# Kernel optimization log

Hardware: AMD Instinct MI355X
Metric: run time of the kernel (lower is better)

The kernel has to match this reference:

```python
import jax, jax.numpy as jnp
import numpy as np

EMB_DIM, D_H, BSZ, SEQ = 2048, 128, 4, 4096
HALF = D_H // 2


def apply_rope(x, sin, cos):
    # x: [b, s, d]; sin/cos: [s, d//2]; interleaved-pair rotation
    b, s, d = x.shape
    xr = x.reshape(b, s, d // 2, 2)
    x0, x1 = xr[..., 0], xr[..., 1]
    r0 = x0 * cos - x1 * sin
    r1 = x1 * cos + x0 * sin
    return jnp.stack([r0, r1], axis=-1).reshape(b, s, d)


def setup_inputs() -> dict:
    key = jax.random.key(0)
    kx, kq, kk, kv = jax.random.split(key, 4)
    x = jax.random.normal(kx, (BSZ, SEQ, EMB_DIM), dtype=jnp.float32)
    # causal mask (1 = attend, 0 = masked), matching mask[q,:] slicing in source
    mask = jnp.tril(jnp.ones((SEQ, SEQ), dtype=jnp.int32))
    # standard RoPE angle tables: [seq, d_h//2]
    inv_freq = 1.0 / (10000.0 ** (jnp.arange(HALF, dtype=jnp.float32) / HALF))
    angles = jnp.arange(SEQ, dtype=jnp.float32)[:, None] * inv_freq[None, :]
    sin, cos = jnp.sin(angles), jnp.cos(angles)
    scale = 1.0 / np.sqrt(EMB_DIM)
    W_Q = jax.random.normal(kq, (EMB_DIM, D_H), dtype=jnp.float32) * scale
    W_K = jax.random.normal(kk, (EMB_DIM, D_H), dtype=jnp.float32) * scale
    W_V = jax.random.normal(kv, (EMB_DIM, D_H), dtype=jnp.float32) * scale
    return {"x": x, "mask": mask, "sin": sin, "cos": cos,
            "W_Q": W_Q, "W_K": W_K, "W_V": W_V}


def reference(x, mask, sin, cos, W_Q, W_V, W_K):
    # QKV projections
    Q = apply_rope(x @ W_Q, sin, cos)  # [b, s, d_h]
    K = apply_rope(x @ W_K, sin, cos)  # [b, s, d_h]
    V = x @ W_V                        # [b, s, d_h]
    # The source's chunked loop is exactly full masked attention over all K/V.
    scores = jnp.einsum('bqd,bkd->bqk', Q, K) / jnp.sqrt(jnp.float32(D_H))
    scores = jnp.where(mask[None, :, :] == 0, -jnp.inf, scores)
    attn = jax.nn.softmax(scores, axis=-1)
    return jnp.einsum('bqk,bkd->bqd', attn, V)
```

## Files before the change

kernel.cpp:

```cpp
#include <hip/hip_runtime.h>
#include <stdint.h>
#include <stddef.h>

typedef __bf16 bf16;
typedef __bf16 bf16x8 __attribute__((ext_vector_type(8)));
typedef float f32x4 __attribute__((ext_vector_type(4)));
typedef unsigned int uint32x2 __attribute__((ext_vector_type(2)));
typedef unsigned int uint32x4 __attribute__((ext_vector_type(4)));

typedef const __attribute__((address_space(1))) uint32_t GU32;
typedef __attribute__((address_space(3))) uint32_t LU32;

__device__ __forceinline__ f32x4 mfma16(bf16x8 a, bf16x8 b, f32x4 c) {
  return __builtin_amdgcn_mfma_f32_16x16x32_bf16(a, b, c, 0, 0, 0);
}
__device__ __forceinline__ void gload16(const void* g, void* l) {
  __builtin_amdgcn_global_load_lds((GU32*)g, (LU32*)l, 16, 0, 0);
}

__global__ void k_prep(const float* __restrict__ Wq, const float* __restrict__ Wk,
                       const float* __restrict__ Wv, bf16* __restrict__ Wct) {
  int t = blockIdx.x * 256 + threadIdx.x;
  int n = t >> 11, k = t & 2047;
  const float* s = (n < 128) ? Wq : (n < 256) ? Wk : Wv;
  Wct[t] = (bf16)s[k * 128 + (n & 127)];
}

__global__ __launch_bounds__(256, 3) void k_proj(
    const float* __restrict__ x, const float* __restrict__ sint, const float* __restrict__ cost,
    const bf16* __restrict__ Wct, bf16* __restrict__ Qg, bf16* __restrict__ Kg,
    bf16* __restrict__ Vtg) {
  __shared__ __align__(16) uint8_t smem[49152];
  const int tid = threadIdx.x;
  const int lane = tid & 63, w = tid >> 6;
  const int l15 = lane & 15, l16 = lane >> 4;
  const int nb = blockIdx.x % 3, mb = blockIdx.x / 3;
  const int wm = w >> 1, wn = w & 1;
  const int arow = tid >> 2, aj = tid & 3;

  f32x4 acc[2][4] = {};
  f32x4 areg[4];

  const float* abase = x + (size_t)(mb * 64 + arow) * 2048 + aj * 16;

  auto stageB = [&](int buf, int ks) {
    uint8_t* bbm = smem + buf * 24576 + 8192;
    int k0 = ks * 64;
#pragma unroll
    for (int i = 0; i < 4; ++i) {
      int L = i * 4096 + tid * 16;
      int n = L >> 7, cp = (L >> 4) & 7;
      int cc = cp ^ (n & 7);
      const uint8_t* src = (const uint8_t*)Wct + (((nb * 128 + n) * 2048 + k0 + cc * 8) << 1);
      gload16(src, bbm + i * 4096 + w * 1024);
    }
  };
  auto loadA = [&](int ks) {
    const f32x4* p = (const f32x4*)(abase + ks * 64);
#pragma unroll
    for (int i = 0; i < 4; ++i) areg[i] = p[i];
  };
  auto writeA = [&](int buf) {
    uint8_t* ab = smem + buf * 24576;
#pragma unroll
    for (int h = 0; h < 2; ++h) {
      union { bf16 v[8]; uint32x4 u; } pk;
#pragma unroll
      for (int e = 0; e < 8; ++e) pk.v[e] = (bf16)areg[h * 2 + (e >> 2)][e & 3];
      int c = aj * 2 + h;
      *(uint32x4*)(ab + arow * 128 + (((c ^ (arow & 7)) & 7) << 4)) = pk.u;
    }
  };
  auto compute = [&](int buf) {
    uint8_t* ab = smem + buf * 24576;
    uint8_t* bbm = ab + 8192;
#pragma unroll
    for (int kk = 0; kk < 2; ++kk) {
      bf16x8 af[2], bv[4];
#pragma unroll
      for (int mt = 0; mt < 2; ++mt) {
        int ml = wm * 32 + mt * 16 + l15;
        af[mt] = *(const bf16x8*)(ab + ml * 128 + (((kk * 4 + l16) ^ (ml & 7)) << 4));
      }
#pragma unroll
      for (int nt = 0; nt < 4; ++nt) {
        int nl = wn * 64 + nt * 16 + l15;
        bv[nt] = *(const bf16x8*)(bbm + nl * 128 + (((kk * 4 + l16) ^ (nl & 7)) << 4));
      }
#pragma unroll
      for (int mt = 0; mt < 2; ++mt)
#pragma unroll
        for (int nt = 0; nt < 4; ++nt)
          acc[mt][nt] = mfma16(af[mt], bv[nt], acc[mt][nt]);
    }
  };

  stageB(0, 0);
  loadA(0);
  writeA(0);
  __syncthreads();
  for (int ks = 0; ks < 32; ++ks) {
    int cur = ks & 1;
    if (ks + 1 < 32) { stageB(cur ^ 1, ks + 1); loadA(ks + 1); }
    compute(cur);
    if (ks + 1 < 32) writeA(cur ^ 1);
    __syncthreads();
  }

  const int bb = mb >> 6;
#pragma unroll
  for (int mt = 0; mt < 2; ++mt) {
    int gm = mb * 64 + wm * 32 + mt * 16 + l16 * 4;
    int s0 = gm & 4095;
#pragma unroll
    for (int nt = 0; nt < 4; ++nt) {
      int jcol = nb * 128 + wn * 64 + nt * 16 + l15;
      f32x4 v = acc[mt][nt];
      if (jcol < 256) {
        int p = (jcol & 127) >> 1;
        bool even = ((jcol & 1) == 0);
#pragma unroll
        for (int r = 0; r < 4; ++r) {
          float pv = __shfl_xor(v[r], 1);
          int s = s0 + r;
          float cs = cost[s * 64 + p], sn = sint[s * 64 + p];
          float nv = even ? (v[r] * cs - pv * sn) : (v[r] * cs + pv * sn);
          bf16 hb = (bf16)nv;
          if (jcol < 128) Qg[((size_t)(bb << 12) + s) * 128 + jcol] = hb;
          else            Kg[((size_t)(bb << 12) + s) * 128 + jcol - 128] = hb;
        }
      } else {
        int d = jcol - 256;
        union { bf16 h[4]; uint32x2 u; } pk;
#pragma unroll
        for (int r = 0; r < 4; ++r) pk.h[r] = (bf16)v[r];
        *(uint32x2*)((uint8_t*)Vtg + (((size_t)(bb << 7) + d) * 4096 + s0) * 2) = pk.u;
      }
    }
  }
}

__global__ __launch_bounds__(256, 2) void k_attn(
    const bf16* __restrict__ Qg, const bf16* __restrict__ Kg, const bf16* __restrict__ Vtg,
    float* __restrict__ PO, float* __restrict__ ML) {
  __shared__ __align__(16) uint8_t smem[81920];
  const int tid = threadIdx.x;
  const int lane = tid & 63, w = tid >> 6;
  const int l15 = lane & 15, l16 = lane >> 4;

  int gid = blockIdx.x;
  int b = gid / 80, rr = gid % 80;
  int j, c;
  if (rr < 8)       { j = rr;                 c = 0; }
  else if (rr < 24) { j = 8 + ((rr - 8) >> 1);  c = (rr - 8) & 1; }
  else if (rr < 48) { j = 16 + (rr - 24) / 3;   c = (rr - 24) % 3; }
  else              { j = 24 + ((rr - 48) >> 2); c = (rr - 48) & 3; }

  const int q0w = j * 128 + w * 32;
  const int kv_lo = c * 1024;
  const int kv_hi = min((c + 1) * 1024, (j + 1) * 128);
  const int T = (kv_hi - kv_lo) >> 6;

  bf16x8 qf[2][4];
#pragma unroll
  for (int qt = 0; qt < 2; ++qt)
#pragma unroll
    for (int kk = 0; kk < 4; ++kk)
      qf[qt][kk] = *(const bf16x8*)(Qg + ((size_t)(b << 12) + q0w + qt * 16 + l15) * 128 + kk * 32 + l16 * 8);

  f32x4 o[2][8] = {};
  float m_r[2] = {-1e30f, -1e30f};
  float l_r[2] = {0.f, 0.f};
  uint8_t* pb = smem + 65536 + w * 4096;

  auto stage = [&](int t) {
    uint8_t* kb = smem + (t & 1) * 32768;
    uint8_t* vb = kb + 16384;
    int kv0 = kv_lo + t * 64;
#pragma unroll
    for (int i = 0; i < 4; ++i) {
      int L = i * 4096 + tid * 16;
      {
        int kv = L >> 8, cp = (L >> 4) & 15, cc = cp ^ (kv & 7);
        const uint8_t* src = (const uint8_t*)Kg + ((size_t)((b << 12) + kv0 + kv) << 8) + (cc << 4);
        gload16(src, kb + i * 4096 + w * 1024);
      }
      {
        int d = L >> 7, cp = (L >> 4) & 7, cc = cp ^ (d & 7);
        const uint8_t* src = (const uint8_t*)Vtg + ((size_t)(((b << 7) + d) << 12) + kv0 + (cc << 3)) * 2;
        gload16(src, vb + i * 4096 + w * 1024);
      }
    }
  };

  stage(0);
  __syncthreads();

  for (int t = 0; t < T; ++t) {
    if (t + 1 < T) stage(t + 1);
    const int kv0 = kv_lo + t * 64;
    if (kv0 <= q0w + 31) {
      uint8_t* kb = smem + (t & 1) * 32768;
      uint8_t* vb = kb + 16384;
      f32x4 sfr[4][2] = {};
#pragma unroll
      for (int kk = 0; kk < 4; ++kk) {
#pragma unroll
        for (int kvt = 0; kvt < 4; ++kvt) {
          int kvl = kvt * 16 + l15;
          bf16x8 kf = *(const bf16x8*)(kb + (kvl << 8) + (((kk * 4 + l16) ^ (kvl & 7)) << 4));
#pragma unroll
          for (int qt = 0; qt < 2; ++qt)
            sfr[kvt][qt] = mfma16(kf, qf[qt][kk], sfr[kvt][qt]);
        }
      }
      const bool need_mask = (kv0 + 63 > q0w);
      const float scale = 0.08838834764831845f;
#pragma unroll
      for (int qt = 0; qt < 2; ++qt) {
        const int q = q0w + qt * 16 + l15;
        float pvv[4][4];
        float tmax = -1e30f;
#pragma unroll
        for (int kvt = 0; kvt < 4; ++kvt)
#pragma unroll
          for (int r = 0; r < 4; ++r) {
            float sv = sfr[kvt][qt][r] * scale;
            if (need_mask) {
              int kv = kv0 + kvt * 16 + l16 * 4 + r;
              if (kv > q) sv = -1e30f;
            }
            pvv[kvt][r] = sv;
            tmax = fmaxf(tmax, sv);
          }
        tmax = fmaxf(tmax, __shfl_xor(tmax, 16));
        tmax = fmaxf(tmax, __shfl_xor(tmax, 32));
        float mnew = fmaxf(m_r[qt], tmax);
        float corr = __expf(m_r[qt] - mnew);
        m_r[qt] = mnew;
        float rs = 0.f;
#pragma unroll
        for (int kvt = 0; kvt < 4; ++kvt)
#pragma unroll
          for (int r = 0; r < 4; ++r) {
            float p = __expf(pvv[kvt][r] - mnew);
            pvv[kvt][r] = p;
            rs += p;
          }
        rs += __shfl_xor(rs, 16);
        rs += __shfl_xor(rs, 32);
        l_r[qt] = l_r[qt] * corr + rs;
        const int qrow = qt * 16 + l15;
#pragma unroll
        for (int kvt = 0; kvt < 4; ++kvt) {
          union { bf16 h[4]; uint32x2 u; } pk;
#pragma unroll
          for (int r = 0; r < 4; ++r) pk.h[r] = (bf16)pvv[kvt][r];
          int kv2 = kvt * 32 + l16 * 8;
          *(uint32x2*)(pb + qrow * 128 + ((((kv2 >> 4) ^ (qrow & 7)) << 4) | (kv2 & 15))) = pk.u;
        }
#pragma unroll
        for (int r = 0; r < 4; ++r) {
          float cr = __shfl(corr, l16 * 4 + r);
#pragma unroll
          for (int dt = 0; dt < 8; ++dt) o[qt][dt][r] *= cr;
        }
      }
#pragma unroll
      for (int kvb = 0; kvb < 2; ++kvb) {
        bf16x8 pa[2];
#pragma unroll
        for (int qt = 0; qt < 2; ++qt) {
          int qrow = qt * 16 + l15;
          int kv2 = kvb * 64 + l16 * 16;
          pa[qt] = *(const bf16x8*)(pb + qrow * 128 + (((kv2 >> 4) ^ (qrow & 7)) << 4));
        }
#pragma unroll
        for (int dt = 0; dt < 8; ++dt) {
          int d = dt * 16 + l15;
          bf16x8 vf = *(const bf16x8*)(vb + (d << 7) + (((kvb * 4 + l16) ^ (d & 7)) << 4));
#pragma unroll
          for (int qt = 0; qt < 2; ++qt)
            o[qt][dt] = mfma16(pa[qt], vf, o[qt][dt]);
        }
      }
    }
    __syncthreads();
  }

  float* POb = PO + (size_t)((b * 32 + j) * 4 + c) * 16384;
#pragma unroll
  for (int qt = 0; qt < 2; ++qt)
#pragma unroll
    for (int dt = 0; dt < 8; ++dt)
#pragma unroll
      for (int r = 0; r < 4; ++r)
        POb[(w * 32 + qt * 16 + l16 * 4 + r) * 128 + dt * 16 + l15] = o[qt][dt][r];
  float* MLb = ML + (size_t)((b * 32 + j) * 4 + c) * 256;
  if (l16 == 0) {
#pragma unroll
    for (int qt = 0; qt < 2; ++qt) {
      MLb[w * 32 + qt * 16 + l15] = m_r[qt];
      MLb[128 + w * 32 + qt * 16 + l15] = l_r[qt];
    }
  }
}

__global__ void k_combine(const float* __restrict__ PO, const float* __restrict__ ML,
                          float* __restrict__ out) {
  int blk = blockIdx.x;
  int b = blk >> 5, j = blk & 31;
  int nc = 1 + (j >> 3);
  int t = threadIdx.x;
  int q = t >> 1, half = t & 1;
  const float* MLb = ML + (size_t)(b * 32 + j) * 4 * 256;
  float mv[4], lv[4];
  float ms = -1e30f;
  for (int cc = 0; cc < nc; ++cc) {
    mv[cc] = MLb[cc * 256 + q];
    lv[cc] = MLb[cc * 256 + 128 + q];
    ms = fmaxf(ms, mv[cc]);
  }
  float wgt[4];
  float den = 0.f;
  for (int cc = 0; cc < nc; ++cc) { wgt[cc] = __expf(mv[cc] - ms); den += wgt[cc] * lv[cc]; }
  float inv = 1.f / den;
  const float* POb = PO + (size_t)(b * 32 + j) * 4 * 16384 + q * 128 + half * 64;
  float* ob = out + ((size_t)(b << 12) + j * 128 + q) * 128 + half * 64;
  for (int d = 0; d < 64; d += 4) {
    f32x4 a = {0.f, 0.f, 0.f, 0.f};
    for (int cc = 0; cc < nc; ++cc) {
      f32x4 v = *(const f32x4*)(POb + cc * 16384 + d);
      a += v * wgt[cc];
    }
    a *= inv;
    *(f32x4*)(ob + d) = a;
  }
}

extern "C" void kernel_launch(void* const* d_in, const int* in_sizes, int n_in,
                              void* d_out, int out_size, void* d_ws, size_t ws_size,
                              hipStream_t stream) {
  const float* x = (const float*)d_in[0];
  const float* sint = (const float*)d_in[2];
  const float* cost = (const float*)d_in[3];
  const float* Wq = (const float*)d_in[4];
  const float* Wk = (const float*)d_in[5];
  const float* Wv = (const float*)d_in[6];
  uint8_t* ws = (uint8_t*)d_ws;

  bf16* Wct = (bf16*)(ws + 0x0);
  bf16* Qg  = (bf16*)(ws + 0x180000);
  bf16* Kg  = (bf16*)(ws + 0x580000);
  bf16* Vtg = (bf16*)(ws + 0x980000);
  float* PO = (float*)(ws + 0xD80000);
  float* ML = (float*)(ws + 0x2D80000);
  float* out = (float*)d_out;

  hipLaunchKernelGGL(k_prep, dim3(3072), dim3(256), 0, stream, Wq, Wk, Wv, Wct);
  hipLaunchKernelGGL(k_proj, dim3(768), dim3(256), 0, stream, x, sint, cost, Wct, Qg, Kg, Vtg);
  hipLaunchKernelGGL(k_attn, dim3(320), dim3(256), 0, stream, Qg, Kg, Vtg, PO, ML);
  hipLaunchKernelGGL(k_combine, dim3(128), dim3(256), 0, stream, PO, ML, out);
}
```

Measured before the change: 152.9 us.

## Widen projection N-tile to 192 columns and transpose weights via LDS

```diff
diff --git a/kernel.cpp b/kernel.cpp
--- a/kernel.cpp
+++ b/kernel.cpp
@@ -18,40 +18,61 @@
   __builtin_amdgcn_global_load_lds((GU32*)g, (LU32*)l, 16, 0, 0);
 }
 
-__global__ void k_prep(const float* __restrict__ Wq, const float* __restrict__ Wk,
-                       const float* __restrict__ Wv, bf16* __restrict__ Wct) {
-  int t = blockIdx.x * 256 + threadIdx.x;
-  int n = t >> 11, k = t & 2047;
-  const float* s = (n < 128) ? Wq : (n < 256) ? Wk : Wv;
-  Wct[t] = (bf16)s[k * 128 + (n & 127)];
-}
-
-__global__ __launch_bounds__(256, 3) void k_proj(
+__global__ __launch_bounds__(256) void k_prep(const float* __restrict__ Wq,
+                                              const float* __restrict__ Wk,
+                                              const float* __restrict__ Wv,
+                                              bf16* __restrict__ Wct) {
+  __shared__ float tile[64][65];
+  const int tid = threadIdx.x;
+  const int widx = blockIdx.x >> 6, rem = blockIdx.x & 63;
+  const int k0 = (rem >> 1) * 64, n0 = (rem & 1) * 64;
+  const float* W = (widx == 0) ? Wq : (widx == 1) ? Wk : Wv;
+  const int rg = tid >> 4, cq = tid & 15;
+#pragma unroll
+  for (int i = 0; i < 4; ++i) {
+    int krow = i * 16 + rg;
+    f32x4 v = *(const f32x4*)(W + (size_t)(k0 + krow) * 128 + n0 + cq * 4);
+#pragma unroll
+    for (int j = 0; j < 4; ++j) tile[krow][cq * 4 + j] = v[j];
+  }
+  __syncthreads();
+#pragma unroll
+  for (int i = 0; i < 4; ++i) {
+    int nrow = i * 16 + rg;
+    union { bf16 h[4]; uint32x2 u; } pk;
+#pragma unroll
+    for (int j = 0; j < 4; ++j) pk.h[j] = (bf16)tile[cq * 4 + j][nrow];
+    *(uint32x2*)(Wct + (size_t)(widx * 128 + n0 + nrow) * 2048 + k0 + cq * 4) = pk.u;
+  }
+}
+
+__global__ __launch_bounds__(256, 2) void k_proj(
     const float* __restrict__ x, const float* __restrict__ sint, const float* __restrict__ cost,
     const bf16* __restrict__ Wct, bf16* __restrict__ Qg, bf16* __restrict__ Kg,
     bf16* __restrict__ Vtg) {
-  __shared__ __align__(16) uint8_t smem[49152];
+  __shared__ __align__(16) uint8_t smem[65536];
   const int tid = threadIdx.x;
   const int lane = tid & 63, w = tid >> 6;
   const int l15 = lane & 15, l16 = lane >> 4;
-  const int nb = blockIdx.x % 3, mb = blockIdx.x / 3;
+  const int logical = (blockIdx.x & 7) * 64 + (blockIdx.x >> 3);
+  const int nb = logical & 1, mb = logical >> 1;
   const int wm = w >> 1, wn = w & 1;
   const int arow = tid >> 2, aj = tid & 3;
 
-  f32x4 acc[2][4] = {};
+  f32x4 acc[2][6] = {};
   f32x4 areg[4];
 
   const float* abase = x + (size_t)(mb * 64 + arow) * 2048 + aj * 16;
 
   auto stageB = [&](int buf, int ks) {
-    uint8_t* bbm = smem + buf * 24576 + 8192;
+    uint8_t* bbm = smem + buf * 32768 + 8192;
     int k0 = ks * 64;
 #pragma unroll
-    for (int i = 0; i < 4; ++i) {
+    for (int i = 0; i < 6; ++i) {
       int L = i * 4096 + tid * 16;
       int n = L >> 7, cp = (L >> 4) & 7;
       int cc = cp ^ (n & 7);
-      const uint8_t* src = (const uint8_t*)Wct + (((nb * 128 + n) * 2048 + k0 + cc * 8) << 1);
+      const uint8_t* src = (const uint8_t*)Wct + (((size_t)(nb * 192 + n) * 2048 + k0 + cc * 8) << 1);
       gload16(src, bbm + i * 4096 + w * 1024);
     }
   };
@@ -61,7 +82,7 @@
     for (int i = 0; i < 4; ++i) areg[i] = p[i];
   };
   auto writeA = [&](int buf) {
-    uint8_t* ab = smem + buf * 24576;
+    uint8_t* ab = smem + buf * 32768;
 #pragma unroll
     for (int h = 0; h < 2; ++h) {
       union { bf16 v[8]; uint32x4 u; } pk;
@@ -72,25 +93,25 @@
     }
   };
   auto compute = [&](int buf) {
-    uint8_t* ab = smem + buf * 24576;
+    uint8_t* ab = smem + buf * 32768;
     uint8_t* bbm = ab + 8192;
 #pragma unroll
     for (int kk = 0; kk < 2; ++kk) {
-      bf16x8 af[2], bv[4];
+      bf16x8 af[2], bv[6];
 #pragma unroll
       for (int mt = 0; mt < 2; ++mt) {
         int ml = wm * 32 + mt * 16 + l15;
         af[mt] = *(const bf16x8*)(ab + ml * 128 + (((kk * 4 + l16) ^ (ml & 7)) << 4));
       }
 #pragma unroll
-      for (int nt = 0; nt < 4; ++nt) {
-        int nl = wn * 64 + nt * 16 + l15;
+      for (int nt = 0; nt < 6; ++nt) {
+        int nl = wn * 96 + nt * 16 + l15;
         bv[nt] = *(const bf16x8*)(bbm + nl * 128 + (((kk * 4 + l16) ^ (nl & 7)) << 4));
       }
 #pragma unroll
       for (int mt = 0; mt < 2; ++mt)
 #pragma unroll
-        for (int nt = 0; nt < 4; ++nt)
+        for (int nt = 0; nt < 6; ++nt)
           acc[mt][nt] = mfma16(af[mt], bv[nt], acc[mt][nt]);
     }
   };
@@ -107,14 +128,13 @@
     __syncthreads();
   }
 
-  const int bb = mb >> 6;
 #pragma unroll
   for (int mt = 0; mt < 2; ++mt) {
     int gm = mb * 64 + wm * 32 + mt * 16 + l16 * 4;
-    int s0 = gm & 4095;
-#pragma unroll
-    for (int nt = 0; nt < 4; ++nt) {
-      int jcol = nb * 128 + wn * 64 + nt * 16 + l15;
+    int bb = gm >> 12, s0 = gm & 4095;
+#pragma unroll
+    for (int nt = 0; nt < 6; ++nt) {
+      int jcol = nb * 192 + wn * 96 + nt * 16 + l15;
       f32x4 v = acc[mt][nt];
       if (jcol < 256) {
         int p = (jcol & 127) >> 1;
@@ -357,8 +377,8 @@
   float* ML = (float*)(ws + 0x2D80000);
   float* out = (float*)d_out;
 
-  hipLaunchKernelGGL(k_prep, dim3(3072), dim3(256), 0, stream, Wq, Wk, Wv, Wct);
-  hipLaunchKernelGGL(k_proj, dim3(768), dim3(256), 0, stream, x, sint, cost, Wct, Qg, Kg, Vtg);
+  hipLaunchKernelGGL(k_prep, dim3(192), dim3(256), 0, stream, Wq, Wk, Wv, Wct);
+  hipLaunchKernelGGL(k_proj, dim3(512), dim3(256), 0, stream, x, sint, cost, Wct, Qg, Kg, Vtg);
   hipLaunchKernelGGL(k_attn, dim3(320), dim3(256), 0, stream, Qg, Kg, Vtg, PO, ML);
   hipLaunchKernelGGL(k_combine, dim3(128), dim3(256), 0, stream, PO, ML, out);
 }
```

Result: faster. 140.7 us (-8.0%).
